# Kernel tuning notes

Hardware: AMD Instinct MI355X
Metric: run time of the kernel (lower is better)

Reference implementation:

```python
import jax, jax.numpy as jnp
import numpy as np

B, S, D, DS = 32, 1024, 256, 64
M = 3  # modalities: audio, visual, lexical


def setup_inputs() -> dict:
    key = jax.random.key(0)
    ks = jax.random.split(key, 16)
    w = 0.05
    return {
        "x_audio": jax.random.normal(ks[0], (B, S, D), jnp.float32),
        "x_visual": jax.random.normal(ks[1], (B, S, D), jnp.float32),
        "x_lexical": jax.random.normal(ks[2], (B, S, D), jnp.float32),
        "XW": jax.random.normal(ks[3], (M, DS, D), jnp.float32) * w,
        "Xb": jax.random.normal(ks[4], (M, DS), jnp.float32) * w,
        "HW": jax.random.normal(ks[5], (M, DS, DS), jnp.float32) * w,
        "Hb": jax.random.normal(ks[6], (M, DS), jnp.float32) * w,
        "OW": jax.random.normal(ks[7], (M, D, DS), jnp.float32) * w,
        "Ob": jax.random.normal(ks[8], (M, D), jnp.float32) * w,
        "CW": jax.random.normal(ks[9], (M, M, DS, DS), jnp.float32) * w,
        "W1": jax.random.normal(ks[10], (DS, M * DS), jnp.float32) * w,
        "b1": jax.random.normal(ks[11], (DS,), jnp.float32) * w,
        "W2": jax.random.normal(ks[12], (M * M, DS), jnp.float32) * w,
        "b2": jax.random.normal(ks[13], (M * M,), jnp.float32) * w,
        "ln_g": jnp.ones((M, D), jnp.float32),
        "ln_b": jnp.zeros((M, D), jnp.float32),
    }


def _layernorm(x, g, b, eps=1e-5):
    mu = jnp.mean(x, axis=-1, keepdims=True)
    var = jnp.mean(jnp.square(x - mu), axis=-1, keepdims=True)
    return (x - mu) * jax.lax.rsqrt(var + eps) * g + b


def reference(x_audio, x_visual, x_lexical, XW, Xb, HW, Hb, OW, Ob, CW,
              W1, b1, W2, b2, ln_g, ln_b):
    x = jnp.stack([x_audio, x_visual, x_lexical], axis=0)  # [M,B,S,D]
    xs = x.transpose(2, 0, 1, 3)                            # [S,M,B,D]
    mask = 1.0 - jnp.eye(M, dtype=x.dtype)                  # src != tgt

    def step(h, x_t):
        # h: [M,B,DS], x_t: [M,B,D]
        hc = h.transpose(1, 0, 2).reshape(h.shape[1], M * DS)      # [B, M*DS]
        raw = jnp.tanh(hc @ W1.T + b1) @ W2.T + b2                 # [B, M*M]
        attn = jax.nn.softmax(raw.reshape(-1, M, M), axis=-1)      # [B, tgt, src]
        hproj = jnp.einsum('tsde,sbe->tsbd', CW, h)                # [tgt,src,B,DS]
        coupling = jnp.einsum('bts,ts,tsbd->tbd', attn, mask, hproj)
        su = (jnp.einsum('mde,mbe->mbd', HW, h) + Hb[:, None, :]
              + jnp.einsum('mdk,mbk->mbd', XW, x_t) + Xb[:, None, :]
              + coupling)
        h_new = jax.nn.silu(su)                                    # [M,B,DS]
        y = jnp.einsum('mkd,mbd->mbk', OW, h_new) + Ob[:, None, :]  # [M,B,D]
        return h_new, y

    h0 = jnp.zeros((M, x.shape[1], DS), x.dtype)
    _, ys = jax.lax.scan(step, h0, xs)          # [S,M,B,D]
    out = ys.transpose(1, 2, 0, 3) + x          # residual, [M,B,S,D]
    out = _layernorm(out, ln_g[:, None, None, :], ln_b[:, None, None, :])
    return (out[0], out[1], out[2])
```

## Files before the change

kernel.cpp:

```cpp
#include <hip/hip_runtime.h>
#include <math.h>

#define B_  32
#define S_  1024
#define D_  256
#define DS_ 64
#define M_  3
#define MD_ 192

#define BAR_LGKM() asm volatile("s_waitcnt lgkmcnt(0)\n\ts_barrier" ::: "memory")

__device__ __forceinline__ float rl_f32(float v, int lane) {
    return __uint_as_float(__builtin_amdgcn_readlane(__float_as_uint(v), lane));
}

#define L2E_ 1.4426950408889634f
__device__ __forceinline__ float fast_exp(float x) { return exp2f(x * L2E_); }
__device__ __forceinline__ float fast_tanh(float x) {
    float t = exp2f(x * (2.0f * L2E_));
    return 1.0f - 2.0f * __builtin_amdgcn_rcpf(t + 1.0f);
}

typedef float v4f __attribute__((ext_vector_type(4)));

#define ALD4(dst, p, off) \
    asm volatile("global_load_dwordx4 %0, %1, off offset:" #off \
                 : "=v"(dst) : "v"(p))

#define DECL_WSET(P, baseptr) \
    v4f P##00, P##01, P##02, P##03, P##04, P##05, P##06, P##07, \
        P##08, P##09, P##10, P##11, P##12, P##13, P##14, P##15; \
    { const float* _wp = (baseptr); \
      ALD4(P##00, _wp, 0);   ALD4(P##01, _wp, 16);  ALD4(P##02, _wp, 32);  ALD4(P##03, _wp, 48);  \
      ALD4(P##04, _wp, 64);  ALD4(P##05, _wp, 80);  ALD4(P##06, _wp, 96);  ALD4(P##07, _wp, 112); \
      ALD4(P##08, _wp, 128); ALD4(P##09, _wp, 144); ALD4(P##10, _wp, 160); ALD4(P##11, _wp, 176); \
      ALD4(P##12, _wp, 192); ALD4(P##13, _wp, 208); ALD4(P##14, _wp, 224); ALD4(P##15, _wp, 240); \
      asm volatile("s_waitcnt vmcnt(0)" ::: "memory"); }

#define EFMA __builtin_elementwise_fma

#define DOT64_PKV(h4, out) { \
    v4f A0 = W00 * (h4)[0]; \
    v4f A1 = W01 * (h4)[1]; \
    v4f A2 = W02 * (h4)[2]; \
    v4f A3 = W03 * (h4)[3]; \
    A0 = EFMA(W04, (h4)[4],  A0); \
    A1 = EFMA(W05, (h4)[5],  A1); \
    A2 = EFMA(W06, (h4)[6],  A2); \
    A3 = EFMA(W07, (h4)[7],  A3); \
    A0 = EFMA(W08, (h4)[8],  A0); \
    A1 = EFMA(W09, (h4)[9],  A1); \
    A2 = EFMA(W10, (h4)[10], A2); \
    A3 = EFMA(W11, (h4)[11], A3); \
    A0 = EFMA(W12, (h4)[12], A0); \
    A1 = EFMA(W13, (h4)[13], A1); \
    A2 = EFMA(W14, (h4)[14], A2); \
    A3 = EFMA(W15, (h4)[15], A3); \
    v4f T = (A0 + A1) + (A2 + A3); \
    out = (T.x + T.y) + (T.z + T.w); \
}

#define DPP_RED3(A, Bv, C) asm volatile( \
    "v_add_f32 %0, %0, %0 row_shr:1 bound_ctrl:0\n\t" \
    "v_add_f32 %1, %1, %1 row_shr:1 bound_ctrl:0\n\t" \
    "v_add_f32 %2, %2, %2 row_shr:1 bound_ctrl:0\n\t" \
    "v_add_f32 %0, %0, %0 row_shr:2 bound_ctrl:0\n\t" \
    "v_add_f32 %1, %1, %1 row_shr:2 bound_ctrl:0\n\t" \
    "v_add_f32 %2, %2, %2 row_shr:2 bound_ctrl:0\n\t" \
    "v_add_f32 %0, %0, %0 row_shr:4 bound_ctrl:0\n\t" \
    "v_add_f32 %1, %1, %1 row_shr:4 bound_ctrl:0\n\t" \
    "v_add_f32 %2, %2, %2 row_shr:4 bound_ctrl:0\n\t" \
    "v_add_f32 %0, %0, %0 row_shr:8 bound_ctrl:0\n\t" \
    "v_add_f32 %1, %1, %1 row_shr:8 bound_ctrl:0\n\t" \
    "v_add_f32 %2, %2, %2 row_shr:8 bound_ctrl:0\n\t" \
    "v_add_f32 %0, %0, %0 row_bcast:15 row_mask:0xa\n\t" \
    "v_add_f32 %1, %1, %1 row_bcast:15 row_mask:0xa\n\t" \
    "v_add_f32 %2, %2, %2 row_bcast:15 row_mask:0xa\n\t" \
    "v_add_f32 %0, %0, %0 row_bcast:31 row_mask:0xc\n\t" \
    "v_add_f32 %1, %1, %1 row_bcast:31 row_mask:0xc\n\t" \
    "v_add_f32 %2, %2, %2 row_bcast:31 row_mask:0xc" \
    : "+v"(A), "+v"(Bv), "+v"(C))

#define DPP_RED4(A, Bv, C, Dv) asm volatile( \
    "v_add_f32 %0, %0, %0 row_shr:1 bound_ctrl:0\n\t" \
    "v_add_f32 %1, %1, %1 row_shr:1 bound_ctrl:0\n\t" \
    "v_add_f32 %2, %2, %2 row_shr:1 bound_ctrl:0\n\t" \
    "v_add_f32 %3, %3, %3 row_shr:1 bound_ctrl:0\n\t" \
    "v_add_f32 %0, %0, %0 row_shr:2 bound_ctrl:0\n\t" \
    "v_add_f32 %1, %1, %1 row_shr:2 bound_ctrl:0\n\t" \
    "v_add_f32 %2, %2, %2 row_shr:2 bound_ctrl:0\n\t" \
    "v_add_f32 %3, %3, %3 row_shr:2 bound_ctrl:0\n\t" \
    "v_add_f32 %0, %0, %0 row_shr:4 bound_ctrl:0\n\t" \
    "v_add_f32 %1, %1, %1 row_shr:4 bound_ctrl:0\n\t" \
    "v_add_f32 %2, %2, %2 row_shr:4 bound_ctrl:0\n\t" \
    "v_add_f32 %3, %3, %3 row_shr:4 bound_ctrl:0\n\t" \
    "v_add_f32 %0, %0, %0 row_shr:8 bound_ctrl:0\n\t" \
    "v_add_f32 %1, %1, %1 row_shr:8 bound_ctrl:0\n\t" \
    "v_add_f32 %2, %2, %2 row_shr:8 bound_ctrl:0\n\t" \
    "v_add_f32 %3, %3, %3 row_shr:8 bound_ctrl:0\n\t" \
    "v_add_f32 %0, %0, %0 row_bcast:15 row_mask:0xa\n\t" \
    "v_add_f32 %1, %1, %1 row_bcast:15 row_mask:0xa\n\t" \
    "v_add_f32 %2, %2, %2 row_bcast:15 row_mask:0xa\n\t" \
    "v_add_f32 %3, %3, %3 row_bcast:15 row_mask:0xa\n\t" \
    "v_add_f32 %0, %0, %0 row_bcast:31 row_mask:0xc\n\t" \
    "v_add_f32 %1, %1, %1 row_bcast:31 row_mask:0xc\n\t" \
    "v_add_f32 %2, %2, %2 row_bcast:31 row_mask:0xc\n\t" \
    "v_add_f32 %3, %3, %3 row_bcast:31 row_mask:0xc" \
    : "+v"(A), "+v"(Bv), "+v"(C), "+v"(Dv))

__global__ __launch_bounds__(256, 2)
void k1_xproj(const float* __restrict__ xa, const float* __restrict__ xv,
              const float* __restrict__ xl, const float* __restrict__ XW,
              const float* __restrict__ Xb, float* __restrict__ xp)
{
    const int m  = blockIdx.z;
    const int b  = blockIdx.y;
    const int t0 = blockIdx.x * 128;
    const float* __restrict__ xm = (m == 0) ? xa : ((m == 1) ? xv : xl);
    const int tid = threadIdx.x;
    const int q = tid >> 6;
    const int d = tid & 63;

    __shared__ __align__(16) float xs[1024];
    __shared__ float part[4][4][64];

    DECL_WSET(W, XW + ((m * 64 + d) * 256 + q * 64));
    const float xbv = Xb[m * 64 + d];

    for (int g = 0; g < 32; ++g) {
        const int tb = t0 + g * 4;
        reinterpret_cast<v4f*>(xs)[tid] =
            reinterpret_cast<const v4f*>(xm + ((size_t)b * S_ + tb) * D_)[tid];
        __syncthreads();
        #pragma unroll
        for (int tt = 0; tt < 4; ++tt) {
            const v4f* xq = reinterpret_cast<const v4f*>(&xs[tt * 256 + q * 64]);
            float accv;
            DOT64_PKV(xq, accv);
            part[tt][q][d] = accv;
        }
        __syncthreads();
        {
            const int tt = q;
            float ssum = part[tt][0][d] + part[tt][1][d] + part[tt][2][d] + part[tt][3][d] + xbv;
            xp[((size_t)b * S_ + tb + tt) * MD_ + m * 64 + d] = ssum;
        }
    }
}

__global__ __launch_bounds__(384, 1)
void k2_recur(const float* __restrict__ xp, float* __restrict__ hbuf,
              const float* __restrict__ HW, const float* __restrict__ Hb,
              const float* __restrict__ CW, const float* __restrict__ W1,
              const float* __restrict__ b1, const float* __restrict__ W2,
              const float* __restrict__ b2)
{
    const int b    = blockIdx.x;
    const int tid  = threadIdx.x;
    const int w    = tid >> 6;
    const int lane = tid & 63;

    const int  seg     = w >> 1;
    const bool is_tail = (w & 1);
    const int  m       = seg;

    __shared__ __align__(16) float hds[2][MD_];
    __shared__ float parts[12][64];

    if (tid < MD_) hds[0][tid] = 0.f;

    const float* baseA;
    const float* baseB;
    int rowA, rowB;
    if (!is_tail) {
        baseA = (seg == 0) ? (HW + lane * 64)
                           : (CW + ((0 * 3 + seg) * 64 + lane) * 64);
        baseB = (seg == 1) ? (HW + (64 + lane) * 64)
                           : (CW + ((1 * 3 + seg) * 64 + lane) * 64);
        rowA = seg; rowB = 3 + seg;
    } else {
        baseA = (seg == 2) ? (HW + (128 + lane) * 64)
                           : (CW + ((2 * 3 + seg) * 64 + lane) * 64);
        baseB = W1 + lane * MD_ + seg * 64;
        rowA = 6 + seg; rowB = 9 + seg;
    }
    DECL_WSET(W, baseA);
    DECL_WSET(X, baseB);

    float hbv = 0.f, b1v = 0.f;
    float w2r0 = 0.f, w2r1 = 0.f, w2r2 = 0.f, b2v0 = 0.f, b2v1 = 0.f, b2v2 = 0.f;
    float xnext = 0.f;
    if (is_tail) {
        hbv  = Hb[m * 64 + lane];
        b1v  = b1[lane];
        w2r0 = W2[(m * 3 + 0) * 64 + lane];
        w2r1 = W2[(m * 3 + 1) * 64 + lane];
        w2r2 = W2[(m * 3 + 2) * 64 + lane];
        b2v0 = b2[m * 3 + 0]; b2v1 = b2[m * 3 + 1]; b2v2 = b2[m * 3 + 2];
        xnext = xp[((size_t)b * S_) * MD_ + m * 64 + lane];
    }
    const int s1 = (m + 1) % 3, s2 = (m + 2) % 3;
    float hist0 = 0.f, hist1 = 0.f, hist2 = 0.f, hist3 = 0.f;

    __syncthreads();

    for (int t = 0; t < S_; ++t) {
        const int cur = t & 1, nxt = cur ^ 1;

        const float xv = xnext;
        if (is_tail && (t + 1 < S_))
            xnext = xp[((size_t)b * S_ + t + 1) * MD_ + m * 64 + lane];

        const v4f* h4 = reinterpret_cast<const v4f*>(&hds[cur][seg * 64]);
        float accA, accB;
        {
            v4f A0, A1, A2, A3, B0, B1, B2, B3;
            {
                v4f H0 = h4[0], H1 = h4[1], H2 = h4[2], H3 = h4[3];
                A0 = W00 * H0; B0 = X00 * H0;
                A1 = W01 * H1; B1 = X01 * H1;
                A2 = W02 * H2; B2 = X02 * H2;
                A3 = W03 * H3; B3 = X03 * H3;
            }
            {
                v4f H0 = h4[4], H1 = h4[5], H2 = h4[6], H3 = h4[7];
                A0 = EFMA(W04, H0, A0); B0 = EFMA(X04, H0, B0);
                A1 = EFMA(W05, H1, A1); B1 = EFMA(X05, H1, B1);
                A2 = EFMA(W06, H2, A2); B2 = EFMA(X06, H2, B2);
                A3 = EFMA(W07, H3, A3); B3 = EFMA(X07, H3, B3);
            }
            {
                v4f H0 = h4[8], H1 = h4[9], H2 = h4[10], H3 = h4[11];
                A0 = EFMA(W08, H0, A0); B0 = EFMA(X08, H0, B0);
                A1 = EFMA(W09, H1, A1); B1 = EFMA(X09, H1, B1);
                A2 = EFMA(W10, H2, A2); B2 = EFMA(X10, H2, B2);
                A3 = EFMA(W11, H3, A3); B3 = EFMA(X11, H3, B3);
            }
            {
                v4f H0 = h4[12], H1 = h4[13], H2 = h4[14], H3 = h4[15];
                A0 = EFMA(W12, H0, A0); B0 = EFMA(X12, H0, B0);
                A1 = EFMA(W13, H1, A1); B1 = EFMA(X13, H1, B1);
                A2 = EFMA(W14, H2, A2); B2 = EFMA(X14, H2, B2);
                A3 = EFMA(W15, H3, A3); B3 = EFMA(X15, H3, B3);
            }
            v4f TA = (A0 + A1) + (A2 + A3);
            v4f TB = (B0 + B1) + (B2 + B3);
            accA = (TA.x + TA.y) + (TA.z + TA.w);
            accB = (TB.x + TB.y) + (TB.z + TB.w);
        }
        parts[rowA][lane] = accA;
        parts[rowB][lane] = accB;
        BAR_LGKM();

        if (is_tail) {
            float pm  = parts[m * 3 + m][lane];
            float pc1 = parts[m * 3 + s1][lane];
            float pc2 = parts[m * 3 + s2][lane];
            float go1 = parts[9 + s1][lane];
            float go2 = parts[9 + s2][lane];

            float z = fast_tanh(b1v + accB + go1 + go2);
            float p0 = w2r0 * z, p1 = w2r1 * z, p2 = w2r2 * z;
            DPP_RED3(p0, p1, p2);
            float r0 = b2v0 + rl_f32(p0, 63);
            float r1 = b2v1 + rl_f32(p1, 63);
            float r2 = b2v2 + rl_f32(p2, 63);
            float mx  = fmaxf(r0, fmaxf(r1, r2));
            float e0  = fast_exp(r0 - mx);
            float e1  = fast_exp(r1 - mx);
            float e2  = fast_exp(r2 - mx);
            float inv = __builtin_amdgcn_rcpf(e0 + e1 + e2);
            float a1v = ((s1 == 1) ? e1 : (s1 == 2) ? e2 : e0) * inv;
            float a2v = ((s2 == 1) ? e1 : (s2 == 2) ? e2 : e0) * inv;

            float suv = xv + hbv + pm + a1v * pc1 + a2v * pc2;
            float hn  = suv * __builtin_amdgcn_rcpf(1.f + fast_exp(-suv));
            hds[nxt][m * 64 + lane] = hn;

            if      ((t & 3) == 0) hist0 = hn;
            else if ((t & 3) == 1) hist1 = hn;
            else if ((t & 3) == 2) hist2 = hn;
            else {
                hist3 = hn;
                float* dst = hbuf + ((size_t)b * S_ + (t - 3)) * MD_ + m * 64 + lane;
                dst[0 * MD_] = hist0; dst[1 * MD_] = hist1;
                dst[2 * MD_] = hist2; dst[3 * MD_] = hist3;
            }
        }
        BAR_LGKM();
    }
}

__global__ __launch_bounds__(256, 2)
void k3_out(const float* __restrict__ xa, const float* __restrict__ xv,
            const float* __restrict__ xl, const float* __restrict__ hbuf,
            const float* __restrict__ OW, const float* __restrict__ Ob,
            const float* __restrict__ lng, const float* __restrict__ lnb,
            float* __restrict__ out)
{
    const int m  = blockIdx.z;
    const int b  = blockIdx.y;
    const int t0 = blockIdx.x * 128;
    const float* __restrict__ xm = (m == 0) ? xa : ((m == 1) ? xv : xl);
    const int k    = threadIdx.x;
    const int wv   = k >> 6;
    const int lane = k & 63;

    __shared__ __align__(16) float hs[4 * 64];
    __shared__ float psum[16], qsum[16];

    DECL_WSET(W, OW + (m * D_ + k) * DS_);
    const float obv = Ob[m * D_ + k];
    const float gv  = lng[m * D_ + k];
    const float bv  = lnb[m * D_ + k];

    for (int gg = 0; gg < 32; ++gg) {
        const int tb = t0 + gg * 4;
        hs[k] = hbuf[((size_t)b * S_ + tb + (k >> 6)) * MD_ + m * 64 + (k & 63)];
        __syncthreads();

        float v0, v1, v2, v3;
        {
            const v4f* h4 = reinterpret_cast<const v4f*>(&hs[0]);
            float accv; DOT64_PKV(h4, accv);
            v0 = obv + accv + xm[((size_t)b * S_ + tb + 0) * D_ + k];
        }
        {
            const v4f* h4 = reinterpret_cast<const v4f*>(&hs[64]);
            float accv; DOT64_PKV(h4, accv);
            v1 = obv + accv + xm[((size_t)b * S_ + tb + 1) * D_ + k];
        }
        {
            const v4f* h4 = reinterpret_cast<const v4f*>(&hs[128]);
            float accv; DOT64_PKV(h4, accv);
            v2 = obv + accv + xm[((size_t)b * S_ + tb + 2) * D_ + k];
        }
        {
            const v4f* h4 = reinterpret_cast<const v4f*>(&hs[192]);
            float accv; DOT64_PKV(h4, accv);
            v3 = obv + accv + xm[((size_t)b * S_ + tb + 3) * D_ + k];
        }

        float s0 = v0, s1v = v1, s2v = v2, s3 = v3;
        float q0 = v0 * v0, q1 = v1 * v1, q2 = v2 * v2, q3 = v3 * v3;
        DPP_RED4(s0, s1v, s2v, s3);
        DPP_RED4(q0, q1, q2, q3);
        if (lane == 63) {
            psum[wv * 4 + 0] = s0;  psum[wv * 4 + 1] = s1v;
            psum[wv * 4 + 2] = s2v; psum[wv * 4 + 3] = s3;
            qsum[wv * 4 + 0] = q0;  qsum[wv * 4 + 1] = q1;
            qsum[wv * 4 + 2] = q2;  qsum[wv * 4 + 3] = q3;
        }
        __syncthreads();

        const size_t obase = (size_t)m * ((size_t)B_ * S_ * D_) + ((size_t)b * S_ + tb) * D_ + k;
        {
            float ss = psum[0] + psum[4] + psum[8] + psum[12];
            float qq = qsum[0] + qsum[4] + qsum[8] + qsum[12];
            float mu = ss * (1.f / 256.f);
            float var = qq * (1.f / 256.f) - mu * mu;
            float rs = rsqrtf(var + 1e-5f);
            out[obase + 0 * D_] = (v0 - mu) * rs * gv + bv;
        }
        {
            float ss = psum[1] + psum[5] + psum[9] + psum[13];
            float qq = qsum[1] + qsum[5] + qsum[9] + qsum[13];
            float mu = ss * (1.f / 256.f);
            float var = qq * (1.f / 256.f) - mu * mu;
            float rs = rsqrtf(var + 1e-5f);
            out[obase + 1 * D_] = (v1 - mu) * rs * gv + bv;
        }
        {
            float ss = psum[2] + psum[6] + psum[10] + psum[14];
            float qq = qsum[2] + qsum[6] + qsum[10] + qsum[14];
            float mu = ss * (1.f / 256.f);
            float var = qq * (1.f / 256.f) - mu * mu;
            float rs = rsqrtf(var + 1e-5f);
            out[obase + 2 * D_] = (v2 - mu) * rs * gv + bv;
        }
        {
            float ss = psum[3] + psum[7] + psum[11] + psum[15];
            float qq = qsum[3] + qsum[7] + qsum[11] + qsum[15];
            float mu = ss * (1.f / 256.f);
            float var = qq * (1.f / 256.f) - mu * mu;
            float rs = rsqrtf(var + 1e-5f);
            out[obase + 3 * D_] = (v3 - mu) * rs * gv + bv;
        }
    }
}

extern "C" void kernel_launch(void* const* d_in, const int* in_sizes, int n_in,
                              void* d_out, int out_size, void* d_ws, size_t ws_size,
                              hipStream_t stream)
{
    const float* xa  = (const float*)d_in[0];
    const float* xv  = (const float*)d_in[1];
    const float* xl  = (const float*)d_in[2];
    const float* XW  = (const float*)d_in[3];
    const float* Xb  = (const float*)d_in[4];
    const float* HW  = (const float*)d_in[5];
    const float* Hb  = (const float*)d_in[6];
    const float* OW  = (const float*)d_in[7];
    const float* Ob  = (const float*)d_in[8];
    const float* CW  = (const float*)d_in[9];
    const float* W1  = (const float*)d_in[10];
    const float* b1  = (const float*)d_in[11];
    const float* W2  = (const float*)d_in[12];
    const float* b2  = (const float*)d_in[13];
    const float* lng = (const float*)d_in[14];
    const float* lnb = (const float*)d_in[15];
    float* out = (float*)d_out;

    float* xp = (float*)d_ws;
    float* hb = xp + (size_t)B_ * S_ * MD_;

    k1_xproj<<<dim3(8, 32, 3), 256, 0, stream>>>(xa, xv, xl, XW, Xb, xp);
    k2_recur<<<dim3(32), 384, 0, stream>>>(xp, hb, HW, Hb, CW, W1, b1, W2, b2);
    k3_out  <<<dim3(8, 32, 3), 256, 0, stream>>>(xa, xv, xl, hb, OW, Ob, lng, lnb, out);
}
```

Before: 1.395 ms.

## Split recurrence dot products across twice as many waves in k2_recur

The recurrent kernel now runs with 768 threads instead of 384. Each wave handles half of the 64-element reduction, holding 32 weights per matrix instead of 64, and partial sums are combined through shared memory by three designated tail waves. The x-projection prefetch also looks two steps ahead instead of one. The aim is to shorten the per-step serial dependency chain of the latency-bound scan, at the cost of more LDS traffic and more waves taking part in each barrier.

After: 1.312 ms. -5.9%, faster.

```diff
diff --git a/kernel.cpp b/kernel.cpp
--- a/kernel.cpp
+++ b/kernel.cpp
@@ -35,6 +35,13 @@
       ALD4(P##04, _wp, 64);  ALD4(P##05, _wp, 80);  ALD4(P##06, _wp, 96);  ALD4(P##07, _wp, 112); \
       ALD4(P##08, _wp, 128); ALD4(P##09, _wp, 144); ALD4(P##10, _wp, 160); ALD4(P##11, _wp, 176); \
       ALD4(P##12, _wp, 192); ALD4(P##13, _wp, 208); ALD4(P##14, _wp, 224); ALD4(P##15, _wp, 240); \
+      asm volatile("s_waitcnt vmcnt(0)" ::: "memory"); }
+
+#define DECL_WSET8(P, baseptr) \
+    v4f P##0, P##1, P##2, P##3, P##4, P##5, P##6, P##7; \
+    { const float* _wp = (baseptr); \
+      ALD4(P##0, _wp, 0);  ALD4(P##1, _wp, 16); ALD4(P##2, _wp, 32); ALD4(P##3, _wp, 48); \
+      ALD4(P##4, _wp, 64); ALD4(P##5, _wp, 80); ALD4(P##6, _wp, 96); ALD4(P##7, _wp, 112); \
       asm volatile("s_waitcnt vmcnt(0)" ::: "memory"); }
 
 #define EFMA __builtin_elementwise_fma
@@ -148,7 +155,7 @@
     }
 }
 
-__global__ __launch_bounds__(384, 1)
+__global__ __launch_bounds__(768, 1)
 void k2_recur(const float* __restrict__ xp, float* __restrict__ hbuf,
               const float* __restrict__ HW, const float* __restrict__ Hb,
               const float* __restrict__ CW, const float* __restrict__ W1,
@@ -160,46 +167,51 @@
     const int w    = tid >> 6;
     const int lane = tid & 63;
 
-    const int  seg     = w >> 1;
-    const bool is_tail = (w & 1);
-    const int  m       = seg;
+    const int seg   = w >> 2;
+    const int rem   = w & 3;
+    const int hh    = rem >> 1;
+    const int which = rem & 1;
+
+    const bool is_tail = (w == 0) | (w == 5) | (w == 10);
+    const int  mm      = (w == 0) ? 0 : ((w == 5) ? 1 : 2);
 
     __shared__ __align__(16) float hds[2][MD_];
-    __shared__ float parts[12][64];
+    __shared__ float parts[12][2][64];
 
     if (tid < MD_) hds[0][tid] = 0.f;
 
     const float* baseA;
     const float* baseB;
     int rowA, rowB;
-    if (!is_tail) {
-        baseA = (seg == 0) ? (HW + lane * 64)
-                           : (CW + ((0 * 3 + seg) * 64 + lane) * 64);
-        baseB = (seg == 1) ? (HW + (64 + lane) * 64)
-                           : (CW + ((1 * 3 + seg) * 64 + lane) * 64);
-        rowA = seg; rowB = 3 + seg;
+    if (which == 0) {
+        baseA = ((seg == 0) ? (HW + lane * 64)
+                            : (CW + ((0 * 3 + seg) * 64 + lane) * 64)) + hh * 32;
+        baseB = ((seg == 1) ? (HW + (64 + lane) * 64)
+                            : (CW + ((1 * 3 + seg) * 64 + lane) * 64)) + hh * 32;
+        rowA = 0 * 3 + seg; rowB = 1 * 3 + seg;
     } else {
-        baseA = (seg == 2) ? (HW + (128 + lane) * 64)
-                           : (CW + ((2 * 3 + seg) * 64 + lane) * 64);
-        baseB = W1 + lane * MD_ + seg * 64;
-        rowA = 6 + seg; rowB = 9 + seg;
+        baseA = ((seg == 2) ? (HW + (128 + lane) * 64)
+                            : (CW + ((2 * 3 + seg) * 64 + lane) * 64)) + hh * 32;
+        baseB = W1 + lane * MD_ + seg * 64 + hh * 32;
+        rowA = 2 * 3 + seg; rowB = 9 + seg;
     }
-    DECL_WSET(W, baseA);
-    DECL_WSET(X, baseB);
+    DECL_WSET8(WA, baseA);
+    DECL_WSET8(WB, baseB);
 
     float hbv = 0.f, b1v = 0.f;
     float w2r0 = 0.f, w2r1 = 0.f, w2r2 = 0.f, b2v0 = 0.f, b2v1 = 0.f, b2v2 = 0.f;
-    float xnext = 0.f;
+    float xn0 = 0.f, xn1 = 0.f;
     if (is_tail) {
-        hbv  = Hb[m * 64 + lane];
+        hbv  = Hb[mm * 64 + lane];
         b1v  = b1[lane];
-        w2r0 = W2[(m * 3 + 0) * 64 + lane];
-        w2r1 = W2[(m * 3 + 1) * 64 + lane];
-        w2r2 = W2[(m * 3 + 2) * 64 + lane];
-        b2v0 = b2[m * 3 + 0]; b2v1 = b2[m * 3 + 1]; b2v2 = b2[m * 3 + 2];
-        xnext = xp[((size_t)b * S_) * MD_ + m * 64 + lane];
+        w2r0 = W2[(mm * 3 + 0) * 64 + lane];
+        w2r1 = W2[(mm * 3 + 1) * 64 + lane];
+        w2r2 = W2[(mm * 3 + 2) * 64 + lane];
+        b2v0 = b2[mm * 3 + 0]; b2v1 = b2[mm * 3 + 1]; b2v2 = b2[mm * 3 + 2];
+        xn0 = xp[((size_t)b * S_ + 0) * MD_ + mm * 64 + lane];
+        xn1 = xp[((size_t)b * S_ + 1) * MD_ + mm * 64 + lane];
     }
-    const int s1 = (m + 1) % 3, s2 = (m + 2) % 3;
+    const int s1 = (mm + 1) % 3, s2 = (mm + 2) % 3;
     float hist0 = 0.f, hist1 = 0.f, hist2 = 0.f, hist3 = 0.f;
 
     __syncthreads();
@@ -207,59 +219,40 @@
     for (int t = 0; t < S_; ++t) {
         const int cur = t & 1, nxt = cur ^ 1;
 
-        const float xv = xnext;
-        if (is_tail && (t + 1 < S_))
-            xnext = xp[((size_t)b * S_ + t + 1) * MD_ + m * 64 + lane];
-
-        const v4f* h4 = reinterpret_cast<const v4f*>(&hds[cur][seg * 64]);
-        float accA, accB;
-        {
-            v4f A0, A1, A2, A3, B0, B1, B2, B3;
-            {
-                v4f H0 = h4[0], H1 = h4[1], H2 = h4[2], H3 = h4[3];
-                A0 = W00 * H0; B0 = X00 * H0;
-                A1 = W01 * H1; B1 = X01 * H1;
-                A2 = W02 * H2; B2 = X02 * H2;
-                A3 = W03 * H3; B3 = X03 * H3;
-            }
-            {
-                v4f H0 = h4[4], H1 = h4[5], H2 = h4[6], H3 = h4[7];
-                A0 = EFMA(W04, H0, A0); B0 = EFMA(X04, H0, B0);
-                A1 = EFMA(W05, H1, A1); B1 = EFMA(X05, H1, B1);
-                A2 = EFMA(W06, H2, A2); B2 = EFMA(X06, H2, B2);
-                A3 = EFMA(W07, H3, A3); B3 = EFMA(X07, H3, B3);
-            }
-            {
-                v4f H0 = h4[8], H1 = h4[9], H2 = h4[10], H3 = h4[11];
-                A0 = EFMA(W08, H0, A0); B0 = EFMA(X08, H0, B0);
-                A1 = EFMA(W09, H1, A1); B1 = EFMA(X09, H1, B1);
-                A2 = EFMA(W10, H2, A2); B2 = EFMA(X10, H2, B2);
-                A3 = EFMA(W11, H3, A3); B3 = EFMA(X11, H3, B3);
-            }
-            {
-                v4f H0 = h4[12], H1 = h4[13], H2 = h4[14], H3 = h4[15];
-                A0 = EFMA(W12, H0, A0); B0 = EFMA(X12, H0, B0);
-                A1 = EFMA(W13, H1, A1); B1 = EFMA(X13, H1, B1);
-                A2 = EFMA(W14, H2, A2); B2 = EFMA(X14, H2, B2);
-                A3 = EFMA(W15, H3, A3); B3 = EFMA(X15, H3, B3);
-            }
-            v4f TA = (A0 + A1) + (A2 + A3);
-            v4f TB = (B0 + B1) + (B2 + B3);
-            accA = (TA.x + TA.y) + (TA.z + TA.w);
-            accB = (TB.x + TB.y) + (TB.z + TB.w);
-        }
-        parts[rowA][lane] = accA;
-        parts[rowB][lane] = accB;
+        const float xv = xn0;
+        xn0 = xn1;
+        if (is_tail && (t + 2 < S_))
+            xn1 = xp[((size_t)b * S_ + t + 2) * MD_ + mm * 64 + lane];
+
+        {
+            const v4f* h4 = reinterpret_cast<const v4f*>(&hds[cur][seg * 64 + hh * 32]);
+            v4f H0 = h4[0], H1 = h4[1], H2 = h4[2], H3 = h4[3];
+            v4f H4 = h4[4], H5 = h4[5], H6 = h4[6], H7 = h4[7];
+            v4f A0 = WA0 * H0, A1 = WA1 * H1;
+            v4f B0 = WB0 * H0, B1 = WB1 * H1;
+            A0 = EFMA(WA2, H2, A0); A1 = EFMA(WA3, H3, A1);
+            B0 = EFMA(WB2, H2, B0); B1 = EFMA(WB3, H3, B1);
+            A0 = EFMA(WA4, H4, A0); A1 = EFMA(WA5, H5, A1);
+            B0 = EFMA(WB4, H4, B0); B1 = EFMA(WB5, H5, B1);
+            A0 = EFMA(WA6, H6, A0); A1 = EFMA(WA7, H7, A1);
+            B0 = EFMA(WB6, H6, B0); B1 = EFMA(WB7, H7, B1);
+            v4f TA = A0 + A1;
+            v4f TB = B0 + B1;
+            parts[rowA][hh][lane] = (TA.x + TA.y) + (TA.z + TA.w);
+            parts[rowB][hh][lane] = (TB.x + TB.y) + (TB.z + TB.w);
+        }
         BAR_LGKM();
 
         if (is_tail) {
-            float pm  = parts[m * 3 + m][lane];
-            float pc1 = parts[m * 3 + s1][lane];
-            float pc2 = parts[m * 3 + s2][lane];
-            float go1 = parts[9 + s1][lane];
-            float go2 = parts[9 + s2][lane];
-
-            float z = fast_tanh(b1v + accB + go1 + go2);
+            float pm  = parts[mm * 3 + mm][0][lane] + parts[mm * 3 + mm][1][lane];
+            float pc1 = parts[mm * 3 + s1][0][lane] + parts[mm * 3 + s1][1][lane];
+            float pc2 = parts[mm * 3 + s2][0][lane] + parts[mm * 3 + s2][1][lane];
+            float ga  = b1v
+                      + (parts[9][0][lane]  + parts[9][1][lane])
+                      + (parts[10][0][lane] + parts[10][1][lane])
+                      + (parts[11][0][lane] + parts[11][1][lane]);
+
+            float z = fast_tanh(ga);
             float p0 = w2r0 * z, p1 = w2r1 * z, p2 = w2r2 * z;
             DPP_RED3(p0, p1, p2);
             float r0 = b2v0 + rl_f32(p0, 63);
@@ -275,14 +268,14 @@
 
             float suv = xv + hbv + pm + a1v * pc1 + a2v * pc2;
             float hn  = suv * __builtin_amdgcn_rcpf(1.f + fast_exp(-suv));
-            hds[nxt][m * 64 + lane] = hn;
+            hds[nxt][mm * 64 + lane] = hn;
 
             if      ((t & 3) == 0) hist0 = hn;
             else if ((t & 3) == 1) hist1 = hn;
             else if ((t & 3) == 2) hist2 = hn;
             else {
                 hist3 = hn;
-                float* dst = hbuf + ((size_t)b * S_ + (t - 3)) * MD_ + m * 64 + lane;
+                float* dst = hbuf + ((size_t)b * S_ + (t - 3)) * MD_ + mm * 64 + lane;
                 dst[0 * MD_] = hist0; dst[1 * MD_] = hist1;
                 dst[2 * MD_] = hist2; dst[3 * MD_] = hist3;
             }
@@ -415,6 +408,6 @@
     float* hb = xp + (size_t)B_ * S_ * MD_;
 
     k1_xproj<<<dim3(8, 32, 3), 256, 0, stream>>>(xa, xv, xl, XW, Xb, xp);
-    k2_recur<<<dim3(32), 384, 0, stream>>>(xp, hb, HW, Hb, CW, W1, b1, W2, b2);
+    k2_recur<<<dim3(32), 768, 0, stream>>>(xp, hb, HW, Hb, CW, W1, b1, W2, b2);
     k3_out  <<<dim3(8, 32, 3), 256, 0, stream>>>(xa, xv, xl, hb, OW, Ob, lng, lnb, out);
 }
```
